# Kernel tuning notes

Hardware: AMD Instinct MI355X
Metric: run time of the kernel (lower is better)

## Reference

```python
import jax, jax.numpy as jnp
import numpy as np

NUM_ENTITIES = 100000
BATCH_SIZE = 4096
E_STATIC = 250000
E_NEW = 4096
D_ENT = 128
D_REL = 64
N_REL = 9
N_TYPES = 3
N_INTENTS = 8
NUM_LAYERS = 3
SCALE = 0.05


def _make_edges(key, n):
    ks = jax.random.split(key, 5)
    src = jax.random.randint(ks[0], (n,), 0, NUM_ENTITIES, dtype=jnp.int32)
    st = jax.random.randint(ks[1], (n,), 0, N_TYPES, dtype=jnp.int32)
    tgt = jax.random.randint(ks[2], (n,), 0, NUM_ENTITIES, dtype=jnp.int32)
    tt = jax.random.randint(ks[3], (n,), 0, N_TYPES, dtype=jnp.int32)
    rel = jax.random.randint(ks[4], (n,), 0, N_REL, dtype=jnp.int32)
    return jnp.stack([src, st, tgt, tt, rel], axis=1)


def setup_inputs() -> dict:
    key = jax.random.key(0)
    ks = jax.random.split(key, 16)
    return {
        'new_edges': _make_edges(ks[0], E_NEW),
        'new_node_types': jax.random.randint(ks[1], (BATCH_SIZE,), 0, N_TYPES, dtype=jnp.int32),
        'static_edges': _make_edges(ks[2], E_STATIC),
        'entity_embeddings': SCALE * jax.random.normal(ks[3], (NUM_ENTITIES - BATCH_SIZE, D_ENT), jnp.float32),
        'default_emb': SCALE * jax.random.normal(ks[4], (N_TYPES, D_ENT), jnp.float32),
        'relation_emb': SCALE * jax.random.normal(ks[5], (N_REL, D_REL), jnp.float32),
        'W_rel': SCALE * jax.random.normal(ks[6], (N_REL, D_ENT, D_REL), jnp.float32),
        'b_rel': SCALE * jax.random.normal(ks[7], (N_REL, D_REL), jnp.float32),
        'W_msg': SCALE * jax.random.normal(ks[8], (N_REL, D_ENT, D_ENT), jnp.float32),
        'W_intent': SCALE * jax.random.normal(ks[9], (N_TYPES, D_ENT, N_INTENTS), jnp.float32),
        'b_intent': SCALE * jax.random.normal(ks[10], (N_TYPES, N_INTENTS), jnp.float32),
        'W_ibn': SCALE * jax.random.normal(ks[11], (N_TYPES, N_INTENTS, N_REL), jnp.float32),
        'b_ibn': SCALE * jax.random.normal(ks[12], (N_TYPES, N_REL), jnp.float32),
    }


def multi_dense(lookups, values, W, b=None, act=None):
    # Same math as tf.gather(W, lookups) followed by values @ w, but computed
    # against all D (<=9) weight slices then selected, to avoid materializing
    # a [E, d_in, d_out] gathered-weights tensor.
    out_all = jnp.einsum('ei,dio->edo', values, W)  # [E, D, d_out]
    out = jnp.take_along_axis(out_all, lookups[:, None, None], axis=1)[:, 0]
    if b is not None:
        out = out + b[lookups]
    return act(out) if act is not None else out


def reference(new_edges, new_node_types, static_edges, entity_embeddings,
              default_emb, relation_emb, W_rel, b_rel, W_msg,
              W_intent, b_intent, W_ibn, b_ibn):
    edges = jnp.concatenate([new_edges, static_edges], axis=0)  # [E, 5]
    sources = edges[:, 0]
    targets = edges[:, 2]
    target_types = edges[:, 3]
    relations = edges[:, 4]

    rel_e = relation_emb[relations]  # [E, D_REL]
    # first BATCH_SIZE entity slots come from type default embeddings
    ent = jnp.concatenate([default_emb[new_node_types], entity_embeddings], axis=0)  # [N, D_ENT]

    layer_edge_weights = []
    for _ in range(NUM_LAYERS):
        src = ent[sources]  # [E, D_ENT]
        tgt = ent[targets]  # [E, D_ENT]
        # per-target intent distribution and per-relation intent weights
        intents = multi_dense(target_types, tgt, W_intent, b_intent, jax.nn.softmax)  # [E, N_INTENTS]
        rel_w = multi_dense(target_types, intents, W_ibn, b_ibn, jax.nn.softmax)  # [E, N_REL]
        iw = jnp.take_along_axis(rel_w, relations[:, None], axis=1)[:, 0]  # [E]
        # per-relation transform of source embeddings
        src_rel = multi_dense(relations, src, W_rel, b_rel, jax.nn.selu)  # [E, D_REL]
        scores = jnp.einsum('er,er,e->e', src_rel, rel_e, iw)  # [E]
        exp_s = jnp.exp(scores)
        denom = jax.ops.segment_sum(exp_s, targets, num_segments=NUM_ENTITIES)  # [N]
        # tf.math.reciprocal_no_nan semantics
        safe = jnp.where(denom != 0, denom, 1.0)
        recip = jnp.where(denom != 0, 1.0 / safe, 0.0)
        dist = exp_s * recip[targets]  # scatter-softmax over incoming edges
        # inference: dropout is identity
        msg = dist[:, None] * multi_dense(relations, src, W_msg, None, None)  # [E, D_ENT]
        ent = jax.ops.segment_sum(msg, targets, num_segments=NUM_ENTITIES)  # [N, D_ENT]
        layer_edge_weights.append(dist)

    return ent, jnp.stack(layer_edge_weights)  # [N, D_ENT], [L, E]
```

## Files before the change

kernel.cpp:

```cpp
#include <hip/hip_runtime.h>
#include <cstddef>
#include <cstdint>

#define NE 100000
#define EN 4096
#define ET 254096
#define D 128
#define DR 64
#define NR 9
#define NT 3
#define NI 8
#define TE 256
#define TILES_X 28

using frag  = __attribute__((ext_vector_type(8))) short;
using f32x4 = __attribute__((ext_vector_type(4))) float;

__device__ __forceinline__ ushort f2b(float x) {
  union { float f; uint32_t u; } v; v.f = x;
  uint32_t r = v.u + 0x7FFFu + ((v.u >> 16) & 1u);
  return (ushort)(r >> 16);
}

__device__ __forceinline__ frag lds_rd(const ushort* b, int row, int k) {
  const int ch = ((k >> 3) ^ (row & 7));
  return *(const frag*)(b + row * D + (ch << 3));
}
__device__ __forceinline__ void lds_wr(ushort* b, int row, int ch, frag v) {
  *(frag*)(b + row * D + ((ch ^ (row & 7)) << 3)) = v;
}
__device__ __forceinline__ void lds_wr2(ushort* b, int row, int k, uint32_t v) {
  const int ch = (k >> 3) ^ (row & 7);
  *(uint32_t*)(b + row * D + (ch << 3) + (k & 7)) = v;
}

__global__ void fill_zero(float4* __restrict__ p, int n4) {
  int i = blockIdx.x * blockDim.x + threadIdx.x;
  if (i < n4) p[i] = make_float4(0.f, 0.f, 0.f, 0.f);
}

__global__ void k_init(ushort* __restrict__ entb, const int* __restrict__ ntypes,
                       const float* __restrict__ def, const float* __restrict__ emb) {
  int i = blockIdx.x * blockDim.x + threadIdx.x;
  if (i >= NE * (D / 4)) return;
  int row = i >> 5, ch = i & 31;
  float4 v;
  if (row < EN) v = ((const float4*)(def + ntypes[row] * D))[ch];
  else v = ((const float4*)(emb + (size_t)(row - EN) * D))[ch];
  ushort4 h;
  h.x = f2b(v.x); h.y = f2b(v.y); h.z = f2b(v.z); h.w = f2b(v.w);
  ((ushort4*)entb)[i] = h;
}

__global__ void k_zero_cnt(int* cnt) { if (threadIdx.x < 48) cnt[threadIdx.x] = 0; }

__global__ __launch_bounds__(256) void k_hist(const int* __restrict__ nedg,
                                              const int* __restrict__ sedg,
                                              int* __restrict__ cnt) {
  __shared__ int h[NR];
  if (threadIdx.x < NR) h[threadIdx.x] = 0;
  __syncthreads();
  int e = blockIdx.x * 256 + threadIdx.x;
  if (e < ET) {
    const int* p = (e < EN) ? nedg + (size_t)e * 5 : sedg + (size_t)(e - EN) * 5;
    atomicAdd(&h[p[4]], 1);
  }
  __syncthreads();
  if (threadIdx.x < NR && h[threadIdx.x]) atomicAdd(&cnt[threadIdx.x], h[threadIdx.x]);
}

__global__ void k_prefix(const int* __restrict__ cnt, int* __restrict__ base,
                         int* __restrict__ head) {
  if (threadIdx.x == 0) {
    int acc = 0;
    for (int r = 0; r < NR; r++) { base[r] = acc; head[r] = acc; acc += cnt[r]; }
  }
}

__global__ __launch_bounds__(256) void k_scatter2(const int* __restrict__ nedg,
                                                  const int* __restrict__ sedg,
                                                  int* __restrict__ head,
                                                  int* __restrict__ bucket) {
  __shared__ int h[NR], bb[NR];
  if (threadIdx.x < NR) h[threadIdx.x] = 0;
  __syncthreads();
  int e = blockIdx.x * 256 + threadIdx.x;
  int r = -1, pos = 0;
  if (e < ET) {
    const int* p = (e < EN) ? nedg + (size_t)e * 5 : sedg + (size_t)(e - EN) * 5;
    r = p[4];
    pos = atomicAdd(&h[r], 1);
  }
  __syncthreads();
  if (threadIdx.x < NR)
    bb[threadIdx.x] = h[threadIdx.x] ? atomicAdd(&head[threadIdx.x], h[threadIdx.x]) : 0;
  __syncthreads();
  if (r >= 0) bucket[bb[r] + pos] = e;
}

__global__ __launch_bounds__(256) void k_thist(const int* __restrict__ nedg,
                                               const int* __restrict__ sedg,
                                               int* __restrict__ thist) {
  int e = blockIdx.x * 256 + threadIdx.x;
  if (e >= ET) return;
  const int* p = (e < EN) ? nedg + (size_t)e * 5 : sedg + (size_t)(e - EN) * 5;
  atomicAdd(&thist[p[2]], 1);
}

__global__ __launch_bounds__(256) void k_scan1(const int* __restrict__ hist,
                                               int* __restrict__ local_ex,
                                               int* __restrict__ bsum, int n) {
  __shared__ int s[256];
  int i = blockIdx.x * 256 + threadIdx.x;
  int v = (i < n) ? hist[i] : 0;
  s[threadIdx.x] = v;
  __syncthreads();
  for (int off = 1; off < 256; off <<= 1) {
    int t = (threadIdx.x >= off) ? s[threadIdx.x - off] : 0;
    __syncthreads();
    s[threadIdx.x] += t;
    __syncthreads();
  }
  if (i < n) local_ex[i] = s[threadIdx.x] - v;
  if (threadIdx.x == 255) bsum[blockIdx.x] = s[255];
}

__global__ __launch_bounds__(512) void k_scan2(int* __restrict__ bsum, int nb) {
  __shared__ int s[512];
  int v = (threadIdx.x < nb) ? bsum[threadIdx.x] : 0;
  s[threadIdx.x] = v;
  __syncthreads();
  for (int off = 1; off < 512; off <<= 1) {
    int t = (threadIdx.x >= off) ? s[threadIdx.x - off] : 0;
    __syncthreads();
    s[threadIdx.x] += t;
    __syncthreads();
  }
  if (threadIdx.x < nb) bsum[threadIdx.x] = s[threadIdx.x] - v;
}

__global__ void k_scan3(int* __restrict__ tgt_off, const int* __restrict__ bsum,
                        int* __restrict__ thead) {
  int i = blockIdx.x * 256 + threadIdx.x;
  if (i < NE) {
    int v = tgt_off[i] + bsum[i >> 8];
    tgt_off[i] = v;
    thead[i] = v;
  }
  if (i == 0) tgt_off[NE] = ET;
}

__global__ __launch_bounds__(256) void k_tscatter(const int* __restrict__ nedg,
                                                  const int* __restrict__ sedg,
                                                  int* __restrict__ thead,
                                                  int* __restrict__ tpos,
                                                  int* __restrict__ esorted) {
  int e = blockIdx.x * 256 + threadIdx.x;
  if (e >= ET) return;
  const int* p = (e < EN) ? nedg + (size_t)e * 5 : sedg + (size_t)(e - EN) * 5;
  int pos = atomicAdd(&thead[p[2]], 1);
  tpos[e] = pos;
  esorted[pos] = e;
}

__global__ __launch_bounds__(1024) void k_pass1(
    const ushort* __restrict__ entb,
    const int* __restrict__ nedg, const int* __restrict__ sedg,
    const int* __restrict__ cnt, const int* __restrict__ base_g,
    const int* __restrict__ bucket, const int* __restrict__ tpos,
    const float* __restrict__ rel_emb,
    const float* __restrict__ W_rel, const float* __restrict__ b_rel,
    const float* __restrict__ W_msg,
    const float* __restrict__ W_int, const float* __restrict__ b_int,
    const float* __restrict__ W_ibn, const float* __restrict__ b_ibn,
    ushort* __restrict__ msgbuf, float* __restrict__ exps_s) {
  const int r = blockIdx.y;
  __shared__ ushort sA[TE * D];
  __shared__ ushort sWm[D * D];
  __shared__ ushort sWr[DR * D];
  __shared__ ushort sWi[NT * 16 * D];
  __shared__ float sInt[TE][NI + 1];
  __shared__ int sS[TE], sT[TE], sTT[TE], sTP[TE];
  __shared__ float sIW[TE];
  __shared__ float sbrel[DR], srele[DR];
  __shared__ float sbint[NT * NI], sWibn[NT * NI * NR], sbibn[NT * NR];

  const int tid = threadIdx.x;
  const int lane = tid & 63;
  const int wv = tid >> 6;
  const int g = lane >> 4;
  const int c = lane & 15;

  const float* Wr = W_rel + (size_t)r * D * DR;
  for (int i = tid; i < (D / 2) * DR; i += 1024) {
    int k2 = i / DR, n = i % DR;
    float a = Wr[(2 * k2) * DR + n], b = Wr[(2 * k2 + 1) * DR + n];
    lds_wr2(sWr, n, 2 * k2, (uint32_t)f2b(a) | ((uint32_t)f2b(b) << 16));
  }
  const float* Wm = W_msg + (size_t)r * D * D;
  for (int i = tid; i < (D / 2) * D; i += 1024) {
    int k2 = i >> 7, n = i & 127;
    float a = Wm[(2 * k2) * D + n], b = Wm[(2 * k2 + 1) * D + n];
    lds_wr2(sWm, n, 2 * k2, (uint32_t)f2b(a) | ((uint32_t)f2b(b) << 16));
  }
  for (int i = tid; i < NT * NI * (D / 2); i += 1024) {
    int tt = i / (NI * D / 2), rem = i % (NI * D / 2), j = rem / (D / 2), k2 = rem % (D / 2);
    const float* Wi = W_int + (size_t)tt * D * NI;
    float a = Wi[(2 * k2) * NI + j], b = Wi[(2 * k2 + 1) * NI + j];
    lds_wr2(sWi, tt * 16 + j, 2 * k2, (uint32_t)f2b(a) | ((uint32_t)f2b(b) << 16));
  }
  for (int i = tid; i < NT * 8 * (D / 2); i += 1024) {
    int tt = i / (8 * D / 2), rem = i % (8 * D / 2), j = rem / (D / 2), k2 = rem % (D / 2);
    lds_wr2(sWi, tt * 16 + 8 + j, 2 * k2, 0u);
  }
  if (tid < DR) { sbrel[tid] = b_rel[r * DR + tid]; srele[tid] = rel_emb[r * DR + tid]; }
  for (int i = tid; i < NT * NI; i += 1024) sbint[i] = b_int[i];
  for (int i = tid; i < NT * NI * NR; i += 1024) sWibn[i] = W_ibn[i];
  for (int i = tid; i < NT * NR; i += 1024) sbibn[i] = b_ibn[i];

  const int nr = cnt[r];
  const int bbase = base_g[r];
  const int ntiles = (nr + TE - 1) / TE;

  for (int tile = blockIdx.x; tile < ntiles; tile += gridDim.x) {
    const int e0 = tile * TE;
    const int ne = min(TE, nr - e0);
    __syncthreads();

    int my_tt = 0;
    if (tid < TE) {
      int s = 0, t = 0, tt = 0, tp = 0;
      if (tid < ne) {
        int eg = bucket[bbase + e0 + tid];
        const int* p = (eg < EN) ? nedg + (size_t)eg * 5 : sedg + (size_t)(eg - EN) * 5;
        s = p[0]; t = p[2]; tt = p[3];
        tp = tpos[eg];
      }
      sS[tid] = s; sT[tid] = t; sTT[tid] = tt; sTP[tid] = tp;
      my_tt = tt;
    }
    __syncthreads();

    {
      const int row = tid & 255, h = tid >> 8;
      const frag* rp = (const frag*)(entb + (size_t)sT[row] * D);
#pragma unroll
      for (int j = 0; j < 4; j++) lds_wr(sA, row, h * 4 + j, rp[h * 4 + j]);
    }
    __syncthreads();

    {
      f32x4 accI[NT];
#pragma unroll
      for (int tt = 0; tt < NT; tt++) accI[tt] = (f32x4){0.f, 0.f, 0.f, 0.f};
#pragma unroll
      for (int ks = 0; ks < 4; ks++) {
        const int k = ks * 32 + g * 8;
        frag a0 = lds_rd(sA, wv * 16 + c, k);
#pragma unroll
        for (int tt = 0; tt < NT; tt++) {
          frag b = lds_rd(sWi, tt * 16 + c, k);
          accI[tt] = __builtin_amdgcn_mfma_f32_16x16x32_bf16(a0, b, accI[tt], 0, 0, 0);
        }
      }
      if (c < NI) {
        const int mb = wv * 16 + g * 4;
#pragma unroll
        for (int tt = 0; tt < NT; tt++)
#pragma unroll
          for (int q = 0; q < 4; q++)
            if (sTT[mb + q] == tt) sInt[mb + q][c] = accI[tt][q];
      }
    }
    __syncthreads();

    {
      const int row = tid & 255, h = tid >> 8;
      const frag* rp = (const frag*)(entb + (size_t)sS[row] * D);
      frag tmp[4];
#pragma unroll
      for (int j = 0; j < 4; j++) tmp[j] = rp[h * 4 + j];

      if (tid < ne) {
        const int tt = my_tt;
        float it[NI], mx = -1e30f;
#pragma unroll
        for (int j = 0; j < NI; j++) {
          it[j] = sInt[tid][j] + sbint[tt * NI + j];
          mx = fmaxf(mx, it[j]);
        }
        float ssum = 0.f;
#pragma unroll
        for (int j = 0; j < NI; j++) { it[j] = __expf(it[j] - mx); ssum += it[j]; }
        const float inv = 1.f / ssum;
        float qv[NR];
#pragma unroll
        for (int k = 0; k < NR; k++) qv[k] = sbibn[tt * NR + k];
#pragma unroll
        for (int j = 0; j < NI; j++) {
          const float ij = it[j] * inv;
#pragma unroll
          for (int k = 0; k < NR; k++) qv[k] = fmaf(ij, sWibn[(tt * NI + j) * NR + k], qv[k]);
        }
        float m9 = qv[0];
#pragma unroll
        for (int k = 1; k < NR; k++) m9 = fmaxf(m9, qv[k]);
        float s9 = 0.f;
#pragma unroll
        for (int k = 0; k < NR; k++) s9 += __expf(qv[k] - m9);
        sIW[tid] = __expf(qv[r] - m9) / s9;
      }
#pragma unroll
      for (int j = 0; j < 4; j++) lds_wr(sA, row, h * 4 + j, tmp[j]);
    }
    __syncthreads();

    f32x4 accR[4], accM[8];
#pragma unroll
    for (int nt = 0; nt < 4; nt++) accR[nt] = (f32x4){0.f, 0.f, 0.f, 0.f};
#pragma unroll
    for (int nt = 0; nt < 8; nt++) accM[nt] = (f32x4){0.f, 0.f, 0.f, 0.f};
#pragma unroll
    for (int ks = 0; ks < 4; ks++) {
      const int k = ks * 32 + g * 8;
      frag a0 = lds_rd(sA, wv * 16 + c, k);
#pragma unroll
      for (int nt = 0; nt < 4; nt++) {
        frag b = lds_rd(sWr, nt * 16 + c, k);
        accR[nt] = __builtin_amdgcn_mfma_f32_16x16x32_bf16(a0, b, accR[nt], 0, 0, 0);
      }
#pragma unroll
      for (int nt = 0; nt < 8; nt++) {
        frag b = lds_rd(sWm, nt * 16 + c, k);
        accM[nt] = __builtin_amdgcn_mfma_f32_16x16x32_bf16(a0, b, accM[nt], 0, 0, 0);
      }
    }

    float es[4];
    {
      float v[4] = {0.f, 0.f, 0.f, 0.f};
#pragma unroll
      for (int nt = 0; nt < 4; nt++) {
        const int col = nt * 16 + c;
        const float br = sbrel[col], re = srele[col];
#pragma unroll
        for (int q = 0; q < 4; q++) {
          const float x = accR[nt][q] + br;
          const float sl = x > 0.f ? 1.0507009873554805f * x
                                   : 1.7580993408473766f * expm1f(x);
          v[q] = fmaf(sl, re, v[q]);
        }
      }
#pragma unroll
      for (int off = 1; off < 16; off <<= 1)
#pragma unroll
        for (int q = 0; q < 4; q++) v[q] += __shfl_xor(v[q], off, 64);
      const int mb = wv * 16 + g * 4;
#pragma unroll
      for (int q = 0; q < 4; q++) {
        const int m = mb + q;
        const float e_s = __expf(v[q] * sIW[m]);
        es[q] = e_s;
        if (c == 0 && m < ne) exps_s[sTP[m]] = e_s;
      }
    }

    {
      const int mb = wv * 16 + g * 4;
#pragma unroll
      for (int q = 0; q < 4; q++) {
        const int m = mb + q;
        ushort* mrow = msgbuf + (size_t)sTP[m] * D;
#pragma unroll
        for (int nt = 0; nt < 8; nt++) {
          float val = accM[nt][q] * es[q];
          float other = __shfl_xor(val, 1, 64);
          if (!(c & 1) && m < ne) {
            uint32_t pk = (uint32_t)f2b(val) | ((uint32_t)f2b(other) << 16);
            *(uint32_t*)(mrow + nt * 16 + c) = pk;
          }
        }
      }
    }
  }
}

__global__ __launch_bounds__(256) void k_agg(
    const ushort* __restrict__ msgbuf, const float* __restrict__ exps_s,
    const int* __restrict__ tgt_off, const int* __restrict__ esorted,
    ushort* __restrict__ entb, float* __restrict__ fout,
    float* __restrict__ dout, int last) {
  const int lg = threadIdx.x & 15;
  const int grp = threadIdx.x >> 4;
  const int ngrp = gridDim.x * 16;
  for (int t = blockIdx.x * 16 + grp; t < NE; t += ngrp) {
    const int beg = tgt_off[t], end = tgt_off[t + 1];
    float a[8] = {0.f, 0.f, 0.f, 0.f, 0.f, 0.f, 0.f, 0.f};
    float dsum = 0.f;
    for (int j = beg; j < end; j++) {
      const uint4 pk = *(const uint4*)(msgbuf + (size_t)j * D + lg * 8);
      dsum += exps_s[j];
      a[0] += __uint_as_float(pk.x << 16); a[1] += __uint_as_float(pk.x & 0xFFFF0000u);
      a[2] += __uint_as_float(pk.y << 16); a[3] += __uint_as_float(pk.y & 0xFFFF0000u);
      a[4] += __uint_as_float(pk.z << 16); a[5] += __uint_as_float(pk.z & 0xFFFF0000u);
      a[6] += __uint_as_float(pk.w << 16); a[7] += __uint_as_float(pk.w & 0xFFFF0000u);
    }
    const float rec = (dsum != 0.f) ? 1.f / dsum : 0.f;
#pragma unroll
    for (int i = 0; i < 8; i++) a[i] *= rec;
    if (last) {
      float4* o = (float4*)(fout + (size_t)t * D + lg * 8);
      o[0] = make_float4(a[0], a[1], a[2], a[3]);
      o[1] = make_float4(a[4], a[5], a[6], a[7]);
    } else {
      uint4 pk;
      pk.x = (uint32_t)f2b(a[0]) | ((uint32_t)f2b(a[1]) << 16);
      pk.y = (uint32_t)f2b(a[2]) | ((uint32_t)f2b(a[3]) << 16);
      pk.z = (uint32_t)f2b(a[4]) | ((uint32_t)f2b(a[5]) << 16);
      pk.w = (uint32_t)f2b(a[6]) | ((uint32_t)f2b(a[7]) << 16);
      *(uint4*)(entb + (size_t)t * D + lg * 8) = pk;
    }
    for (int j = beg + lg; j < end; j += 16) dout[esorted[j]] = exps_s[j] * rec;
  }
}

extern "C" void kernel_launch(void* const* d_in, const int* in_sizes, int n_in,
                              void* d_out, int out_size, void* d_ws, size_t ws_size,
                              hipStream_t stream) {
  const int* nedg = (const int*)d_in[0];
  const int* ntypes = (const int*)d_in[1];
  const int* sedg = (const int*)d_in[2];
  const float* emb = (const float*)d_in[3];
  const float* def = (const float*)d_in[4];
  const float* rel_emb = (const float*)d_in[5];
  const float* W_rel = (const float*)d_in[6];
  const float* b_rel = (const float*)d_in[7];
  const float* W_msg = (const float*)d_in[8];
  const float* W_int = (const float*)d_in[9];
  const float* b_int = (const float*)d_in[10];
  const float* W_ibn = (const float*)d_in[11];
  const float* b_ibn = (const float*)d_in[12];
  float* out = (float*)d_out;

  char* w = (char*)d_ws;
  size_t off = 0;
  ushort* entb = (ushort*)(w + off); off += (size_t)NE * D * 2;
  ushort* msgbuf = (ushort*)(w + off); off += (size_t)ET * D * 2;
  float* exps_s = (float*)(w + off); off += (size_t)ET * 4;
  int* bucket = (int*)(w + off); off += (size_t)ET * 4;
  int* tpos = (int*)(w + off); off += (size_t)ET * 4;
  int* esorted = (int*)(w + off); off += (size_t)ET * 4;
  int* tgt_off = (int*)(w + off); off += (size_t)(NE + 4) * 4;
  int* thead = (int*)(w + off); off += (size_t)NE * 4;
  int* thist = (int*)(w + off); off += (size_t)NE * 4;
  int* bsum = (int*)(w + off); off += 2048;
  int* cnt = (int*)(w + off); off += 64;
  int* base_g = cnt + 16;
  int* head = cnt + 32;
  float* dist_base = out + (size_t)NE * D;

  const int eblocks = (ET + 255) / 256;
  const int nb = (NE + 255) / 256;

  k_init<<<dim3((NE * (D / 4) + 255) / 256), 256, 0, stream>>>(entb, ntypes, def, emb);
  k_zero_cnt<<<1, 64, 0, stream>>>(cnt);
  k_hist<<<dim3(eblocks), 256, 0, stream>>>(nedg, sedg, cnt);
  k_prefix<<<1, 64, 0, stream>>>(cnt, base_g, head);
  k_scatter2<<<dim3(eblocks), 256, 0, stream>>>(nedg, sedg, head, bucket);

  fill_zero<<<dim3((NE / 4 + 255) / 256), 256, 0, stream>>>((float4*)thist, NE / 4);
  k_thist<<<dim3(eblocks), 256, 0, stream>>>(nedg, sedg, thist);
  k_scan1<<<dim3(nb), 256, 0, stream>>>(thist, tgt_off, bsum, NE);
  k_scan2<<<1, 512, 0, stream>>>(bsum, nb);
  k_scan3<<<dim3(nb), 256, 0, stream>>>(tgt_off, bsum, thead);
  k_tscatter<<<dim3(eblocks), 256, 0, stream>>>(nedg, sedg, thead, tpos, esorted);

  for (int l = 0; l < 3; l++) {
    k_pass1<<<dim3(TILES_X, NR), 1024, 0, stream>>>(
        entb, nedg, sedg, cnt, base_g, bucket, tpos, rel_emb, W_rel, b_rel, W_msg,
        W_int, b_int, W_ibn, b_ibn, msgbuf, exps_s);
    k_agg<<<dim3(2048), 256, 0, stream>>>(msgbuf, exps_s, tgt_off, esorted, entb, out,
                                          dist_base + (size_t)l * ET, l == 2);
  }
}
```

Before: 375.8 us.

## Precompute per-entity intent relation weights in a separate kernel before each layer

Adds a per-layer kernel that computes, for every entity and every target type, the intent softmax and relation-weight softmax once, storing a [NE,3,9] table. The edge pass then looks up its weight by (target, type, relation) instead of gathering target embeddings and running an intent MFMA plus softmax per edge. This removes a target-row gather, two barriers and LDS staging per tile. The cost is a full-entity pass over 100k rows each layer. It also swaps manual bf16 rounding for the packed v_cvt_pk_bf16_f32 instruction and uses __expf-1 instead of expm1f in SELU.

After: 399.2 us. +6.2%, slower.

```diff
diff --git a/kernel.cpp b/kernel.cpp
--- a/kernel.cpp
+++ b/kernel.cpp
@@ -20,6 +20,12 @@
   union { float f; uint32_t u; } v; v.f = x;
   uint32_t r = v.u + 0x7FFFu + ((v.u >> 16) & 1u);
   return (ushort)(r >> 16);
+}
+
+__device__ __forceinline__ uint32_t cvtpk(float lo, float hi) {
+  uint32_t r;
+  asm("v_cvt_pk_bf16_f32 %0, %1, %2" : "=v"(r) : "v"(lo), "v"(hi));
+  return r;
 }
 
 __device__ __forceinline__ frag lds_rd(const ushort* b, int row, int k) {
@@ -163,27 +169,127 @@
   esorted[pos] = e;
 }
 
+__global__ __launch_bounds__(256) void k_iw(
+    const ushort* __restrict__ entb,
+    const float* __restrict__ W_int, const float* __restrict__ b_int,
+    const float* __restrict__ W_ibn, const float* __restrict__ b_ibn,
+    float* __restrict__ IW) {
+  __shared__ ushort sE[TE * D];
+  __shared__ ushort sWi[NT * 16 * D];
+  __shared__ float sInt3[TE * 25];
+  __shared__ float sbint[NT * NI], sWibn[NT * NI * NR], sbibn[NT * NR];
+
+  const int tid = threadIdx.x;
+  const int lane = tid & 63, wv = tid >> 6, g = lane >> 4, c = lane & 15;
+
+  for (int i = tid; i < NT * NI * (D / 2); i += 256) {
+    int tt = i / (NI * D / 2), rem = i % (NI * D / 2), j = rem / (D / 2), k2 = rem % (D / 2);
+    const float* Wi = W_int + (size_t)tt * D * NI;
+    lds_wr2(sWi, tt * 16 + j, 2 * k2, cvtpk(Wi[(2 * k2) * NI + j], Wi[(2 * k2 + 1) * NI + j]));
+  }
+  for (int i = tid; i < NT * 8 * (D / 2); i += 256) {
+    int tt = i / (8 * D / 2), rem = i % (8 * D / 2), j = rem / (D / 2), k2 = rem % (D / 2);
+    lds_wr2(sWi, tt * 16 + 8 + j, 2 * k2, 0u);
+  }
+  for (int i = tid; i < NT * NI; i += 256) sbint[i] = b_int[i];
+  for (int i = tid; i < NT * NI * NR; i += 256) sWibn[i] = W_ibn[i];
+  for (int i = tid; i < NT * NR; i += 256) sbibn[i] = b_ibn[i];
+
+  const int ebase = blockIdx.x * TE;
+  for (int i = tid; i < TE * 16; i += 256) {
+    int row = i >> 4, ch = i & 15;
+    int ent = ebase + row;
+    frag v = {};
+    if (ent < NE) v = ((const frag*)(entb + (size_t)ent * D))[ch];
+    lds_wr(sE, row, ch, v);
+  }
+  __syncthreads();
+
+  f32x4 accI[4][NT];
+#pragma unroll
+  for (int mt = 0; mt < 4; mt++)
+#pragma unroll
+    for (int tt = 0; tt < NT; tt++) accI[mt][tt] = (f32x4){0.f, 0.f, 0.f, 0.f};
+#pragma unroll
+  for (int ks = 0; ks < 4; ks++) {
+    const int k = ks * 32 + g * 8;
+    frag b[NT];
+#pragma unroll
+    for (int tt = 0; tt < NT; tt++) b[tt] = lds_rd(sWi, tt * 16 + c, k);
+#pragma unroll
+    for (int mt = 0; mt < 4; mt++) {
+      frag a = lds_rd(sE, (wv * 4 + mt) * 16 + c, k);
+#pragma unroll
+      for (int tt = 0; tt < NT; tt++)
+        accI[mt][tt] = __builtin_amdgcn_mfma_f32_16x16x32_bf16(a, b[tt], accI[mt][tt], 0, 0, 0);
+    }
+  }
+  if (c < NI) {
+#pragma unroll
+    for (int mt = 0; mt < 4; mt++) {
+      const int rb = (wv * 4 + mt) * 16 + g * 4;
+#pragma unroll
+      for (int tt = 0; tt < NT; tt++)
+#pragma unroll
+        for (int q = 0; q < 4; q++) sInt3[(rb + q) * 25 + tt * 8 + c] = accI[mt][tt][q];
+    }
+  }
+  __syncthreads();
+
+  const int ent = ebase + tid;
+  if (ent < NE) {
+    float* outp = IW + (size_t)ent * NT * NR;
+#pragma unroll
+    for (int tt = 0; tt < NT; tt++) {
+      float it[NI], mx = -1e30f;
+#pragma unroll
+      for (int j = 0; j < NI; j++) {
+        it[j] = sInt3[tid * 25 + tt * 8 + j] + sbint[tt * NI + j];
+        mx = fmaxf(mx, it[j]);
+      }
+      float ssum = 0.f;
+#pragma unroll
+      for (int j = 0; j < NI; j++) { it[j] = __expf(it[j] - mx); ssum += it[j]; }
+      const float inv = 1.f / ssum;
+      float qv[NR];
+#pragma unroll
+      for (int k = 0; k < NR; k++) qv[k] = sbibn[tt * NR + k];
+#pragma unroll
+      for (int j = 0; j < NI; j++) {
+        const float ij = it[j] * inv;
+#pragma unroll
+        for (int k = 0; k < NR; k++) qv[k] = fmaf(ij, sWibn[(tt * NI + j) * NR + k], qv[k]);
+      }
+      float m9 = qv[0];
+#pragma unroll
+      for (int k = 1; k < NR; k++) m9 = fmaxf(m9, qv[k]);
+      float s9 = 0.f;
+#pragma unroll
+      for (int k = 0; k < NR; k++) s9 += __expf(qv[k] - m9);
+      const float i9 = 1.f / s9;
+#pragma unroll
+      for (int k = 0; k < NR; k++) outp[tt * NR + k] = __expf(qv[k] - m9) * i9;
+    }
+  }
+}
+
 __global__ __launch_bounds__(1024) void k_pass1(
     const ushort* __restrict__ entb,
     const int* __restrict__ nedg, const int* __restrict__ sedg,
     const int* __restrict__ cnt, const int* __restrict__ base_g,
     const int* __restrict__ bucket, const int* __restrict__ tpos,
+    const float* __restrict__ IW,
     const float* __restrict__ rel_emb,
     const float* __restrict__ W_rel, const float* __restrict__ b_rel,
     const float* __restrict__ W_msg,
-    const float* __restrict__ W_int, const float* __restrict__ b_int,
-    const float* __restrict__ W_ibn, const float* __restrict__ b_ibn,
     ushort* __restrict__ msgbuf, float* __restrict__ exps_s) {
   const int r = blockIdx.y;
   __shared__ ushort sA[TE * D];
   __shared__ ushort sWm[D * D];
   __shared__ ushort sWr[DR * D];
-  __shared__ ushort sWi[NT * 16 * D];
-  __shared__ float sInt[TE][NI + 1];
-  __shared__ int sS[TE], sT[TE], sTT[TE], sTP[TE];
+  __shared__ int sTP[TE];
   __shared__ float sIW[TE];
   __shared__ float sbrel[DR], srele[DR];
-  __shared__ float sbint[NT * NI], sWibn[NT * NI * NR], sbibn[NT * NR];
 
   const int tid = threadIdx.x;
   const int lane = tid & 63;
@@ -194,29 +300,14 @@
   const float* Wr = W_rel + (size_t)r * D * DR;
   for (int i = tid; i < (D / 2) * DR; i += 1024) {
     int k2 = i / DR, n = i % DR;
-    float a = Wr[(2 * k2) * DR + n], b = Wr[(2 * k2 + 1) * DR + n];
-    lds_wr2(sWr, n, 2 * k2, (uint32_t)f2b(a) | ((uint32_t)f2b(b) << 16));
+    lds_wr2(sWr, n, 2 * k2, cvtpk(Wr[(2 * k2) * DR + n], Wr[(2 * k2 + 1) * DR + n]));
   }
   const float* Wm = W_msg + (size_t)r * D * D;
   for (int i = tid; i < (D / 2) * D; i += 1024) {
     int k2 = i >> 7, n = i & 127;
-    float a = Wm[(2 * k2) * D + n], b = Wm[(2 * k2 + 1) * D + n];
-    lds_wr2(sWm, n, 2 * k2, (uint32_t)f2b(a) | ((uint32_t)f2b(b) << 16));
-  }
-  for (int i = tid; i < NT * NI * (D / 2); i += 1024) {
-    int tt = i / (NI * D / 2), rem = i % (NI * D / 2), j = rem / (D / 2), k2 = rem % (D / 2);
-    const float* Wi = W_int + (size_t)tt * D * NI;
-    float a = Wi[(2 * k2) * NI + j], b = Wi[(2 * k2 + 1) * NI + j];
-    lds_wr2(sWi, tt * 16 + j, 2 * k2, (uint32_t)f2b(a) | ((uint32_t)f2b(b) << 16));
-  }
-  for (int i = tid; i < NT * 8 * (D / 2); i += 1024) {
-    int tt = i / (8 * D / 2), rem = i % (8 * D / 2), j = rem / (D / 2), k2 = rem % (D / 2);
-    lds_wr2(sWi, tt * 16 + 8 + j, 2 * k2, 0u);
+    lds_wr2(sWm, n, 2 * k2, cvtpk(Wm[(2 * k2) * D + n], Wm[(2 * k2 + 1) * D + n]));
   }
   if (tid < DR) { sbrel[tid] = b_rel[r * DR + tid]; srele[tid] = rel_emb[r * DR + tid]; }
-  for (int i = tid; i < NT * NI; i += 1024) sbint[i] = b_int[i];
-  for (int i = tid; i < NT * NI * NR; i += 1024) sWibn[i] = W_ibn[i];
-  for (int i = tid; i < NT * NR; i += 1024) sbibn[i] = b_ibn[i];
 
   const int nr = cnt[r];
   const int bbase = base_g[r];
@@ -227,91 +318,20 @@
     const int ne = min(TE, nr - e0);
     __syncthreads();
 
-    int my_tt = 0;
-    if (tid < TE) {
-      int s = 0, t = 0, tt = 0, tp = 0;
-      if (tid < ne) {
-        int eg = bucket[bbase + e0 + tid];
-        const int* p = (eg < EN) ? nedg + (size_t)eg * 5 : sedg + (size_t)(eg - EN) * 5;
-        s = p[0]; t = p[2]; tt = p[3];
-        tp = tpos[eg];
-      }
-      sS[tid] = s; sT[tid] = t; sTT[tid] = tt; sTP[tid] = tp;
-      my_tt = tt;
-    }
-    __syncthreads();
-
     {
       const int row = tid & 255, h = tid >> 8;
-      const frag* rp = (const frag*)(entb + (size_t)sT[row] * D);
+      int eg = 0;
+      if (row < ne) eg = bucket[bbase + e0 + row];
+      const int* p = (eg < EN) ? nedg + (size_t)eg * 5 : sedg + (size_t)(eg - EN) * 5;
+      const int s = p[0];
+      if (h == 0 && row < ne) {
+        const int t = p[2], tt = p[3];
+        sTP[row] = tpos[eg];
+        sIW[row] = IW[((size_t)t * NT + tt) * NR + r];
+      }
+      const frag* rp = (const frag*)(entb + (size_t)s * D);
 #pragma unroll
       for (int j = 0; j < 4; j++) lds_wr(sA, row, h * 4 + j, rp[h * 4 + j]);
-    }
-    __syncthreads();
-
-    {
-      f32x4 accI[NT];
-#pragma unroll
-      for (int tt = 0; tt < NT; tt++) accI[tt] = (f32x4){0.f, 0.f, 0.f, 0.f};
-#pragma unroll
-      for (int ks = 0; ks < 4; ks++) {
-        const int k = ks * 32 + g * 8;
-        frag a0 = lds_rd(sA, wv * 16 + c, k);
-#pragma unroll
-        for (int tt = 0; tt < NT; tt++) {
-          frag b = lds_rd(sWi, tt * 16 + c, k);
-          accI[tt] = __builtin_amdgcn_mfma_f32_16x16x32_bf16(a0, b, accI[tt], 0, 0, 0);
-        }
-      }
-      if (c < NI) {
-        const int mb = wv * 16 + g * 4;
-#pragma unroll
-        for (int tt = 0; tt < NT; tt++)
-#pragma unroll
-          for (int q = 0; q < 4; q++)
-            if (sTT[mb + q] == tt) sInt[mb + q][c] = accI[tt][q];
-      }
-    }
-    __syncthreads();
-
-    {
-      const int row = tid & 255, h = tid >> 8;
-      const frag* rp = (const frag*)(entb + (size_t)sS[row] * D);
-      frag tmp[4];
-#pragma unroll
-      for (int j = 0; j < 4; j++) tmp[j] = rp[h * 4 + j];
-
-      if (tid < ne) {
-        const int tt = my_tt;
-        float it[NI], mx = -1e30f;
-#pragma unroll
-        for (int j = 0; j < NI; j++) {
-          it[j] = sInt[tid][j] + sbint[tt * NI + j];
-          mx = fmaxf(mx, it[j]);
-        }
-        float ssum = 0.f;
-#pragma unroll
-        for (int j = 0; j < NI; j++) { it[j] = __expf(it[j] - mx); ssum += it[j]; }
-        const float inv = 1.f / ssum;
-        float qv[NR];
-#pragma unroll
-        for (int k = 0; k < NR; k++) qv[k] = sbibn[tt * NR + k];
-#pragma unroll
-        for (int j = 0; j < NI; j++) {
-          const float ij = it[j] * inv;
-#pragma unroll
-          for (int k = 0; k < NR; k++) qv[k] = fmaf(ij, sWibn[(tt * NI + j) * NR + k], qv[k]);
-        }
-        float m9 = qv[0];
-#pragma unroll
-        for (int k = 1; k < NR; k++) m9 = fmaxf(m9, qv[k]);
-        float s9 = 0.f;
-#pragma unroll
-        for (int k = 0; k < NR; k++) s9 += __expf(qv[k] - m9);
-        sIW[tid] = __expf(qv[r] - m9) / s9;
-      }
-#pragma unroll
-      for (int j = 0; j < 4; j++) lds_wr(sA, row, h * 4 + j, tmp[j]);
     }
     __syncthreads();
 
@@ -336,6 +356,8 @@
       }
     }
 
+    const int mb = wv * 16 + g * 4;
+
     float es[4];
     {
       float v[4] = {0.f, 0.f, 0.f, 0.f};
@@ -347,7 +369,7 @@
         for (int q = 0; q < 4; q++) {
           const float x = accR[nt][q] + br;
           const float sl = x > 0.f ? 1.0507009873554805f * x
-                                   : 1.7580993408473766f * expm1f(x);
+                                   : 1.7580993408473766f * (__expf(x) - 1.f);
           v[q] = fmaf(sl, re, v[q]);
         }
       }
@@ -355,18 +377,15 @@
       for (int off = 1; off < 16; off <<= 1)
 #pragma unroll
         for (int q = 0; q < 4; q++) v[q] += __shfl_xor(v[q], off, 64);
-      const int mb = wv * 16 + g * 4;
 #pragma unroll
       for (int q = 0; q < 4; q++) {
         const int m = mb + q;
-        const float e_s = __expf(v[q] * sIW[m]);
-        es[q] = e_s;
-        if (c == 0 && m < ne) exps_s[sTP[m]] = e_s;
+        es[q] = __expf(v[q] * sIW[m]);
+        if (c == 0 && m < ne) exps_s[sTP[m]] = es[q];
       }
     }
 
     {
-      const int mb = wv * 16 + g * 4;
 #pragma unroll
       for (int q = 0; q < 4; q++) {
         const int m = mb + q;
@@ -375,10 +394,8 @@
         for (int nt = 0; nt < 8; nt++) {
           float val = accM[nt][q] * es[q];
           float other = __shfl_xor(val, 1, 64);
-          if (!(c & 1) && m < ne) {
-            uint32_t pk = (uint32_t)f2b(val) | ((uint32_t)f2b(other) << 16);
-            *(uint32_t*)(mrow + nt * 16 + c) = pk;
-          }
+          if (!(c & 1) && m < ne)
+            *(uint32_t*)(mrow + nt * 16 + c) = cvtpk(val, other);
         }
       }
     }
@@ -454,7 +471,8 @@
   int* thead = (int*)(w + off); off += (size_t)NE * 4;
   int* thist = (int*)(w + off); off += (size_t)NE * 4;
   int* bsum = (int*)(w + off); off += 2048;
-  int* cnt = (int*)(w + off); off += 64;
+  int* cnt = (int*)(w + off); off += 192;
+  float* IW = (float*)(w + off); off += (size_t)NE * NT * NR * 4;
   int* base_g = cnt + 16;
   int* head = cnt + 32;
   float* dist_base = out + (size_t)NE * D;
@@ -476,9 +494,10 @@
   k_tscatter<<<dim3(eblocks), 256, 0, stream>>>(nedg, sedg, thead, tpos, esorted);
 
   for (int l = 0; l < 3; l++) {
+    k_iw<<<dim3(nb), 256, 0, stream>>>(entb, W_int, b_int, W_ibn, b_ibn, IW);
     k_pass1<<<dim3(TILES_X, NR), 1024, 0, stream>>>(
-        entb, nedg, sedg, cnt, base_g, bucket, tpos, rel_emb, W_rel, b_rel, W_msg,
-        W_int, b_int, W_ibn, b_ibn, msgbuf, exps_s);
+        entb, nedg, sedg, cnt, base_g, bucket, tpos, IW, rel_emb, W_rel, b_rel, W_msg,
+        msgbuf, exps_s);
     k_agg<<<dim3(2048), 256, 0, stream>>>(msgbuf, exps_s, tgt_off, esorted, entb, out,
                                           dist_base + (size_t)l * ET, l == 2);
   }
```
